# Optimization experiments

Hardware: AMD Instinct MI355X
Metric: run time of the kernel (lower is better)

## Reference

```python
import jax, jax.numpy as jnp
import numpy as np

MIN_PS = 4
MAX_PS = 16


def _enforce(mb):
    # mb: (L,) bool candidate boundaries (merge_signal < 0.7-quantile)
    # Faithful re-implementation of _enforce_patch_size_constraints:
    # walk boundaries left->right, skip segments < MIN_PS (start not advanced),
    # accept otherwise, and insert ceil(ps/MAX_PS)-1 evenly spaced splits for
    # oversized segments. seq_len-1 is always appended as a candidate.
    L = mb.shape[0]
    pos = jnp.arange(L, dtype=jnp.int32)
    cand = mb | (pos == L - 1)

    def fwd_step(start, inp):
        p, is_c = inp
        ps = p - start
        acc = is_c & (ps >= MIN_PS)
        k = jnp.where(acc, (ps + MAX_PS - 1) // MAX_PS, jnp.int32(1))
        sz = jnp.maximum(jnp.where(acc, ps // k, jnp.int32(1)), 1)
        new_start = jnp.where(acc, p, start)
        return new_start, (acc, start, sz, k)

    _, (acc, seg_start, sz, k) = jax.lax.scan(fwd_step, jnp.int32(0), (pos, cand))

    # Reverse scan: propagate each accepted boundary's (start, split_size, num_splits)
    # back to the interior positions of its segment so splits can be placed in parallel.
    def rev_step(carry, inp):
        a, s, z, kk = inp
        cs, cz, ck, cv = carry
        out = (cs, cz, ck, cv)
        ncarry = (jnp.where(a, s, cs), jnp.where(a, z, cz), jnp.where(a, kk, ck), cv | a)
        return ncarry, out

    init = (jnp.int32(0), jnp.int32(1), jnp.int32(1), jnp.bool_(False))
    _, (fs, fz, fk, fv) = jax.lax.scan(rev_step, init, (acc, seg_start, sz, k), reverse=True)
    r = pos - fs
    j = r // fz
    split = fv & (r > 0) & (r % fz == 0) & (j >= 1) & (j <= fk - 1)
    return acc | split


def reference(x, attention_mask, W1, b1, W2, b2, Wc, bc, Wb1, bb1, Wb2, bb2):
    B, L, D = x.shape
    # content scorer: Linear -> ReLU -> Linear -> Sigmoid
    content = jax.nn.sigmoid(jax.nn.relu(x @ W1 + b1) @ W2 + b2)[..., 0]  # (B, L)
    # grouped Conv1d(d, d//2, k=3, pad=1, groups=d//4)
    xc = jnp.transpose(x, (0, 2, 1))  # (B, D, L)
    pf = jax.lax.conv_general_dilated(xc, Wc, (1,), ((1, 1),),
                                      feature_group_count=D // 4,
                                      dimension_numbers=('NCH', 'OIH', 'NCH'))
    pf = jnp.transpose(pf + bc[None, :, None], (0, 2, 1))  # (B, L, D//2)
    comb = jnp.concatenate([x, pf], axis=-1)
    bscore = jax.nn.sigmoid(jax.nn.relu(comb @ Wb1 + bb1) @ Wb2 + bb2)[..., 0]  # (B, L)
    signal = content * (1.0 - bscore) * attention_mask
    thr = jnp.quantile(signal, 0.7, axis=1, keepdims=True)
    mb = signal < thr
    new_b = jax.vmap(_enforce)(mb)  # (B, L) bool, new_b[:,0] is always False

    # segment id per token = inclusive cumsum of boundaries
    seg = jnp.cumsum(new_b.astype(jnp.int32), axis=1)
    seg_flat = (seg + jnp.arange(B, dtype=jnp.int32)[:, None] * L).reshape(-1)
    NS = B * L
    xm = x * attention_mask[..., None]
    e = jnp.sum(xm * xm, axis=-1).reshape(-1)  # softmax logits = ||token||^2
    m = jax.ops.segment_max(e, seg_flat, num_segments=NS)
    w = jnp.exp(e - m[seg_flat])
    denom = jax.ops.segment_sum(w, seg_flat, num_segments=NS)
    wn = w / denom[seg_flat]
    merged = jax.ops.segment_sum(xm.reshape(-1, D) * wn[:, None], seg_flat,
                                 num_segments=NS).reshape(B, L, D)
    # segment_boundaries: 1 for every segment except the first, zero padding
    n_last = seg[:, -1]
    p = jnp.arange(L)
    seg_bounds = ((p[None, :] >= 1) & (p[None, :] <= n_last[:, None])).astype(jnp.float32)
    return merged, seg_bounds


def setup_inputs() -> dict:
    key = jax.random.key(0)
    B, L, D = 4, 8192, 512
    ks = jax.random.split(key, 8)
    s = 0.02
    return {
        'x': jax.random.normal(ks[0], (B, L, D), jnp.float32),
        'attention_mask': jnp.ones((B, L), jnp.float32),
        'W1': jax.random.normal(ks[1], (D, D // 4), jnp.float32) * s,
        'b1': jnp.zeros((D // 4,), jnp.float32),
        'W2': jax.random.normal(ks[2], (D // 4, 1), jnp.float32) * s,
        'b2': jnp.zeros((1,), jnp.float32),
        'Wc': jax.random.normal(ks[3], (D // 2, 4, 3), jnp.float32) * s,
        'bc': jnp.zeros((D // 2,), jnp.float32),
        'Wb1': jax.random.normal(ks[4], (D + D // 2, D // 4), jnp.float32) * s,
        'bb1': jnp.zeros((D // 4,), jnp.float32),
        'Wb2': jax.random.normal(ks[5], (D // 4, 1), jnp.float32) * s,
        'bb2': jnp.zeros((1,), jnp.float32),
    }
```

## Files before the change

### kernel.cpp

```cpp
#include <hip/hip_runtime.h>
#include <math.h>

#define B_  4
#define L_  8192
#define D_  512
#define BL_ (B_*L_)
#define TOK 64
#define XS  68
#define KC  16
#define NCH (D_/KC)

__global__ __launch_bounds__(256, 2) void k_signal(
    const float* __restrict__ x, const float* __restrict__ mask,
    const float* __restrict__ W1, const float* __restrict__ b1,
    const float* __restrict__ W2, const float* __restrict__ b2,
    const float* __restrict__ Wc, const float* __restrict__ bc,
    const float* __restrict__ Wb1, const float* __restrict__ bb1,
    const float* __restrict__ Wb2, const float* __restrict__ bb2,
    float* __restrict__ signal, float* __restrict__ e,
    unsigned int* __restrict__ hist16,
    float* __restrict__ merged, float* __restrict__ bounds)
{
  __shared__ float ws1[KC][128];
  __shared__ float wsb[KC][128];
  __shared__ float wsp[8][128];
  __shared__ float xt[KC][XS];
  __shared__ float pf[8][XS];

  const int t   = threadIdx.x;
  const int blk = blockIdx.x;
  const int b   = blk >> 7;
  const int l0  = (blk & 127) << 6;
  const float* xb = x + (size_t)b * L_ * D_;

  const int jq = t & 31, tw = t >> 5;
  const int j0 = jq << 2, tok0 = tw << 3;

  const int stok = t >> 2, skk = t & 3;
  const int oo_c = t >> 5;
  const int m2   = (t & 31) << 1;
  const int cb_c = (oo_c >> 1) << 2;

  const int srow = t >> 5, sc4 = (t & 31) << 2;

  if (t < 16) {
    float4* bz = reinterpret_cast<float4*>(bounds + (size_t)b * L_ + l0);
    bz[t] = make_float4(0.f, 0.f, 0.f, 0.f);
  }
  float4* mz = reinterpret_cast<float4*>(merged + (size_t)(b * L_ + l0) * D_);

  float a1[8][4], a2[8][4];
#pragma unroll
  for (int i = 0; i < 8; ++i)
#pragma unroll
    for (int j = 0; j < 4; ++j) { a1[i][j] = 0.f; a2[i][j] = 0.f; }
  float esacc = 0.f;

  float4 r_w1a, r_w1b, r_wba, r_wbb, r_wp, r_xv, r_hv;
  float4 r_wc0, r_wc1, r_wc2;
  float  r_bc;

  auto LOAD = [&](int c) {
    const int kc = c << 4;
    r_w1a = *reinterpret_cast<const float4*>(W1  + (size_t)(kc + srow) * 128 + sc4);
    r_w1b = *reinterpret_cast<const float4*>(W1  + (size_t)(kc + 8 + srow) * 128 + sc4);
    r_wba = *reinterpret_cast<const float4*>(Wb1 + (size_t)(kc + srow) * 128 + sc4);
    r_wbb = *reinterpret_cast<const float4*>(Wb1 + (size_t)(kc + 8 + srow) * 128 + sc4);
    r_wp  = *reinterpret_cast<const float4*>(Wb1 + (size_t)(512 + (c << 3) + srow) * 128 + sc4);
    r_xv  = *reinterpret_cast<const float4*>(xb + (size_t)(l0 + stok) * D_ + kc + (skk << 2));
    if (t < 8) {
      const int hh = t >> 2, kk = t & 3;
      const int l = hh ? (l0 + TOK) : (l0 - 1);
      r_hv = make_float4(0.f, 0.f, 0.f, 0.f);
      if (l >= 0 && l < L_)
        r_hv = *reinterpret_cast<const float4*>(xb + (size_t)l * D_ + kc + (kk << 2));
    }
    const int o = (c << 3) + oo_c;
    const float* wcp = Wc + o * 12;
    r_wc0 = *reinterpret_cast<const float4*>(wcp);
    r_wc1 = *reinterpret_cast<const float4*>(wcp + 4);
    r_wc2 = *reinterpret_cast<const float4*>(wcp + 8);
    r_bc  = bc[o];
  };

  LOAD(0);

  for (int c = 0; c < NCH; ++c) {
    __syncthreads();

    *reinterpret_cast<float4*>(&ws1[srow][sc4])     = r_w1a;
    *reinterpret_cast<float4*>(&ws1[8 + srow][sc4]) = r_w1b;
    *reinterpret_cast<float4*>(&wsb[srow][sc4])     = r_wba;
    *reinterpret_cast<float4*>(&wsb[8 + srow][sc4]) = r_wbb;
    *reinterpret_cast<float4*>(&wsp[srow][sc4])     = r_wp;
    {
      const float4 v = r_xv;
      esacc = fmaf(v.x, v.x, esacc); esacc = fmaf(v.y, v.y, esacc);
      esacc = fmaf(v.z, v.z, esacc); esacc = fmaf(v.w, v.w, esacc);
      const int r = skk << 2;
      xt[r + 0][stok] = v.x; xt[r + 1][stok] = v.y;
      xt[r + 2][stok] = v.z; xt[r + 3][stok] = v.w;
    }
    if (t < 8) {
      const int hh = t >> 2, kk = t & 3;
      const int col = TOK + hh, r = kk << 2;
      xt[r + 0][col] = r_hv.x; xt[r + 1][col] = r_hv.y;
      xt[r + 2][col] = r_hv.z; xt[r + 3][col] = r_hv.w;
    }
    __syncthreads();

    float wcl[12];
    wcl[0] = r_wc0.x; wcl[1]  = r_wc0.y; wcl[2]  = r_wc0.z; wcl[3]  = r_wc0.w;
    wcl[4] = r_wc1.x; wcl[5]  = r_wc1.y; wcl[6]  = r_wc1.z; wcl[7]  = r_wc1.w;
    wcl[8] = r_wc2.x; wcl[9]  = r_wc2.y; wcl[10] = r_wc2.z; wcl[11] = r_wc2.w;
    const float bcv = r_bc;

    if (c + 1 < NCH) LOAD(c + 1);

    mz[(c << 8) + t] = make_float4(0.f, 0.f, 0.f, 0.f);

    {
      float pa = bcv, pb = bcv;
      const int tm1 = (m2 == 0) ? TOK : m2 - 1;
      const int tp2 = (m2 + 2 == TOK) ? TOK + 1 : m2 + 2;
#pragma unroll
      for (int i = 0; i < 4; ++i) {
        const float* row = &xt[cb_c + i][0];
        const float  xm1 = row[tm1];
        const float2 x01 = *reinterpret_cast<const float2*>(&row[m2]);
        const float  xp2 = row[tp2];
        pa = fmaf(xm1,   wcl[i * 3 + 0], pa);
        pa = fmaf(x01.x, wcl[i * 3 + 1], pa);
        pa = fmaf(x01.y, wcl[i * 3 + 2], pa);
        pb = fmaf(x01.x, wcl[i * 3 + 0], pb);
        pb = fmaf(x01.y, wcl[i * 3 + 1], pb);
        pb = fmaf(xp2,   wcl[i * 3 + 2], pb);
      }
      *reinterpret_cast<float2*>(&pf[oo_c][m2]) = make_float2(pa, pb);
    }

#pragma unroll 4
    for (int k = 0; k < KC; ++k) {
      const float4 w1 = *reinterpret_cast<const float4*>(&ws1[k][j0]);
      const float4 wb = *reinterpret_cast<const float4*>(&wsb[k][j0]);
      const float4 xa = *reinterpret_cast<const float4*>(&xt[k][tok0]);
      const float4 xc = *reinterpret_cast<const float4*>(&xt[k][tok0 + 4]);
      const float xs8[8] = {xa.x, xa.y, xa.z, xa.w, xc.x, xc.y, xc.z, xc.w};
#pragma unroll
      for (int i = 0; i < 8; ++i) {
        a1[i][0] = fmaf(xs8[i], w1.x, a1[i][0]);
        a1[i][1] = fmaf(xs8[i], w1.y, a1[i][1]);
        a1[i][2] = fmaf(xs8[i], w1.z, a1[i][2]);
        a1[i][3] = fmaf(xs8[i], w1.w, a1[i][3]);
        a2[i][0] = fmaf(xs8[i], wb.x, a2[i][0]);
        a2[i][1] = fmaf(xs8[i], wb.y, a2[i][1]);
        a2[i][2] = fmaf(xs8[i], wb.z, a2[i][2]);
        a2[i][3] = fmaf(xs8[i], wb.w, a2[i][3]);
      }
    }
    __syncthreads();

#pragma unroll 2
    for (int oo = 0; oo < 8; ++oo) {
      const float4 wp = *reinterpret_cast<const float4*>(&wsp[oo][j0]);
      const float4 pa4 = *reinterpret_cast<const float4*>(&pf[oo][tok0]);
      const float4 pb4 = *reinterpret_cast<const float4*>(&pf[oo][tok0 + 4]);
      const float ps8[8] = {pa4.x, pa4.y, pa4.z, pa4.w, pb4.x, pb4.y, pb4.z, pb4.w};
#pragma unroll
      for (int i = 0; i < 8; ++i) {
        a2[i][0] = fmaf(ps8[i], wp.x, a2[i][0]);
        a2[i][1] = fmaf(ps8[i], wp.y, a2[i][1]);
        a2[i][2] = fmaf(ps8[i], wp.z, a2[i][2]);
        a2[i][3] = fmaf(ps8[i], wp.w, a2[i][3]);
      }
    }
  }

  {
    float b1v[4], w2v[4], bbv[4], wv2[4];
#pragma unroll
    for (int jj = 0; jj < 4; ++jj) {
      b1v[jj] = b1[j0 + jj];  w2v[jj] = W2[j0 + jj];
      bbv[jj] = bb1[j0 + jj]; wv2[jj] = Wb2[j0 + jj];
    }
    const float bias2 = b2[0], biasb2 = bb2[0];
#pragma unroll
    for (int i = 0; i < 8; ++i) {
      float p1 = 0.f, p2 = 0.f;
#pragma unroll
      for (int jj = 0; jj < 4; ++jj) {
        const float h1 = a1[i][jj] + b1v[jj];
        if (h1 > 0.f) p1 = fmaf(h1, w2v[jj], p1);
        const float h2 = a2[i][jj] + bbv[jj];
        if (h2 > 0.f) p2 = fmaf(h2, wv2[jj], p2);
      }
#pragma unroll
      for (int off = 1; off < 32; off <<= 1) {
        p1 += __shfl_xor(p1, off, 64);
        p2 += __shfl_xor(p2, off, 64);
      }
      if (jq == 0) {
        const int gi = b * L_ + l0 + tok0 + i;
        const float content = 1.f / (1.f + expf(-(p1 + bias2)));
        const float bscore  = 1.f / (1.f + expf(-(p2 + biasb2)));
        const float s = content * (1.f - bscore) * mask[gi];
        signal[gi] = s;
        const unsigned int u = __float_as_uint(s);
        const unsigned int key = (u & 0x80000000u) ? ~u : (u | 0x80000000u);
        const unsigned int bb16 = key >> 16;
        atomicAdd(&hist16[((unsigned)b << 16) | ((bb16 & 63u) << 10) | (bb16 >> 6)], 1u);
      }
    }
  }

  {
    float es = esacc;
    es += __shfl_xor(es, 1, 64);
    es += __shfl_xor(es, 2, 64);
    if (skk == 0) {
      const int gi = b * L_ + l0 + stok;
      const float m = mask[gi];
      e[gi] = m * m * es;
    }
  }
}

__device__ __forceinline__ int chain_sim(unsigned long long w, int from) {
  int last = -1;
  while (from < 64) {
    const unsigned long long m = w & (~0ull << from);
    if (m == 0ull) break;
    const int p = __ffsll(m) - 1;
    last = p;
    from = p + 4;
  }
  return last;
}

__global__ __launch_bounds__(1024) void k_select(
    const float* __restrict__ signal, const unsigned int* __restrict__ hist16,
    int* __restrict__ starts, int* __restrict__ nlast)
{
  __shared__ unsigned int bins[4][256];
  __shared__ unsigned int sel_prefix;
  __shared__ int sel_rank;
  __shared__ int sel_tt, sel_rr;
  __shared__ unsigned int wpart[16];
  __shared__ float sh_thr;
  __shared__ unsigned int wmin[16];
  __shared__ int wcnt[16];
  __shared__ unsigned long long cw[128];
  __shared__ unsigned char nb[L_];
  __shared__ signed char tbl[128][4];
  __shared__ int st_in[128];
  __shared__ int offs[257];

  const int b = blockIdx.x, t = threadIdx.x;
  const int wv = t >> 6, lane = t & 63;
  const float* s = signal + b * L_;
  const unsigned int* hb = hist16 + ((unsigned)b << 16);

  float val[8];
  unsigned int key[8];
#pragma unroll
  for (int i = 0; i < 8; ++i) {
    val[i] = s[(i << 10) + t];
    const unsigned int u = __float_as_uint(val[i]);
    key[i] = (u & 0x80000000u) ? ~u : (u | 0x80000000u);
  }

  unsigned int tsum = 0;
#pragma unroll 8
  for (int i = 0; i < 64; ++i) tsum += hb[(i << 10) | t];
  {
    unsigned int run = tsum;
#pragma unroll
    for (int off = 1; off < 64; off <<= 1) {
      const unsigned int v = __shfl_up(run, off, 64);
      if (lane >= off) run += v;
    }
    if (lane == 63) wpart[wv] = run;
    __syncthreads();
    unsigned int wadd = 0;
    for (int g = 0; g < wv; ++g) wadd += wpart[g];
    run += wadd;
    const unsigned int excl = run - tsum;
    const int r = 5733;
    if (r >= (int)excl && r < (int)run) { sel_tt = t; sel_rr = r - (int)excl; }
    __syncthreads();
    if (t < 64) {
      const int tt = sel_tt, rr = sel_rr;
      const unsigned int cnt = hb[(t << 10) | tt];
      unsigned int irun = cnt;
#pragma unroll
      for (int off = 1; off < 64; off <<= 1) {
        const unsigned int v = __shfl_up(irun, off, 64);
        if (t >= off) irun += v;
      }
      const unsigned int iexcl = irun - cnt;
      if (rr >= (int)iexcl && rr < (int)irun) {
        sel_prefix = ((unsigned int)tt << 6) | (unsigned int)t;
        sel_rank   = rr - (int)iexcl;
      }
    }
    __syncthreads();
  }

  for (int round = 2; round < 4; ++round) {
    reinterpret_cast<unsigned int*>(bins)[t] = 0u;
    __syncthreads();
    const unsigned int pre = sel_prefix;
    const int shift = 24 - 8 * round;
#pragma unroll
    for (int i = 0; i < 8; ++i) {
      if ((key[i] >> (shift + 8)) == pre)
        atomicAdd(&bins[t >> 8][(key[i] >> shift) & 255u], 1u);
    }
    __syncthreads();
    if (t < 256)
      bins[0][t] = bins[0][t] + bins[1][t] + bins[2][t] + bins[3][t];
    __syncthreads();
    if (t < 64) {
      const unsigned int c0 = bins[0][(t << 2) + 0], c1 = bins[0][(t << 2) + 1];
      const unsigned int c2 = bins[0][(t << 2) + 2], c3 = bins[0][(t << 2) + 3];
      const unsigned int lsum = c0 + c1 + c2 + c3;
      unsigned int run = lsum;
#pragma unroll
      for (int off = 1; off < 64; off <<= 1) {
        const unsigned int v = __shfl_up(run, off, 64);
        if (t >= off) run += v;
      }
      const int r = sel_rank;
      if (r >= (int)(run - lsum) && r < (int)run) {
        int rr = r - (int)(run - lsum);
        unsigned int cbin;
        if (rr < (int)c0) { cbin = 0; }
        else if (rr < (int)(c0 + c1)) { cbin = 1; rr -= (int)c0; }
        else if (rr < (int)(c0 + c1 + c2)) { cbin = 2; rr -= (int)(c0 + c1); }
        else { cbin = 3; rr -= (int)(c0 + c1 + c2); }
        sel_rank = rr;
        sel_prefix = (pre << 8) | ((unsigned int)(t << 2) | cbin);
      }
    }
    __syncthreads();
  }
  const unsigned int k0 = sel_prefix;

  {
    int cle = 0;
    unsigned int mgt = 0xFFFFFFFFu;
#pragma unroll
    for (int i = 0; i < 8; ++i) {
      if (key[i] <= k0) ++cle;
      else mgt = min(mgt, key[i]);
    }
#pragma unroll
    for (int off = 1; off < 64; off <<= 1) {
      cle += __shfl_xor(cle, off, 64);
      mgt = min(mgt, (unsigned int)__shfl_xor((int)mgt, off, 64));
    }
    if (lane == 0) { wcnt[wv] = cle; wmin[wv] = mgt; }
    __syncthreads();
    if (t == 0) {
      int C = 0; unsigned int M = 0xFFFFFFFFu;
      for (int g = 0; g < 16; ++g) { C += wcnt[g]; M = min(M, wmin[g]); }
      const unsigned int k1 = (C >= 5735) ? k0 : M;
      const unsigned int u0 = (k0 & 0x80000000u) ? (k0 & 0x7fffffffu) : ~k0;
      const unsigned int u1 = (k1 & 0x80000000u) ? (k1 & 0x7fffffffu) : ~k1;
      const float v0 = __uint_as_float(u0);
      const float v1 = __uint_as_float(u1);
      const float g = 0.7f * 8191.0f - 5733.0f;
      sh_thr = v0 + g * (v1 - v0);
    }
    __syncthreads();
  }
  const float thr = sh_thr;

#pragma unroll
  for (int i = 0; i < 8; ++i) {
    const unsigned long long m = __ballot(val[i] < thr);
    if (lane == 0) cw[(i << 4) + wv] = m;
  }
  {
    const int base = t << 3;
#pragma unroll
    for (int i = 0; i < 8; ++i) nb[base + i] = 0;
  }
  __syncthreads();
  if (t == 0) cw[127] |= (1ull << 63);
  __syncthreads();

  if (t < 512) {
    const int blk = t >> 2, cls = t & 3;
    tbl[blk][cls] = (signed char)chain_sim(cw[blk], cls);
  }
  __syncthreads();

  if (t == 0) {
    int st = 0;
    for (int blk = 0; blk < 128; ++blk) {
      const int bs = blk << 6;
      st_in[blk] = st;
      int pl;
      if (blk == 0) {
        pl = chain_sim(cw[0], 4);
      } else {
        int off = st + 4 - bs;
        if (off < 0) off = 0;
        pl = tbl[blk][off];
      }
      if (pl >= 0) st = bs + pl;
    }
  }
  __syncthreads();

  if (t < 128) {
    const int bs = t << 6;
    const unsigned long long w = cw[t];
    int st = st_in[t];
    int from = st + 4 - bs;
    if (from < 0) from = 0;
    while (from < 64) {
      const unsigned long long m = w & (~0ull << from);
      if (m == 0ull) break;
      const int p_rel = __ffsll(m) - 1;
      const int p = bs + p_rel;
      nb[p] = 1;
      const int ps = p - st;
      const int k = (ps + 15) >> 4;
      if (k > 1) {
        int sz = ps / k; if (sz < 1) sz = 1;
        for (int j = 1; j < k; ++j) nb[st + j * sz] = 1;
      }
      st = p;
      from = p_rel + 4;
    }
  }
  __syncthreads();

  int ls = 0, run2 = 0;
  if (t < 256) {
    const int base = t << 5;
    for (int i = 0; i < 32; ++i) ls += nb[base + i];
    run2 = ls;
#pragma unroll
    for (int off = 1; off < 64; off <<= 1) {
      const int v = __shfl_up(run2, off, 64);
      if ((t & 63) >= off) run2 += v;
    }
    if ((t & 63) == 63) wcnt[t >> 6] = run2;
  }
  __syncthreads();
  if (t < 256) {
    const int w = t >> 6;
    int addb = 0;
    if (w > 0) addb += wcnt[0];
    if (w > 1) addb += wcnt[1];
    if (w > 2) addb += wcnt[2];
    offs[t] = addb + run2 - ls;
    if (t == 255) offs[256] = addb + run2;
  }
  __syncthreads();
  if (t < 256) {
    const int base = t << 5;
    int rn = offs[t];
    for (int i = 0; i < 32; ++i) {
      rn += nb[base + i];
      if (nb[base + i]) starts[b * L_ + rn] = base + i;
    }
  }
  if (t == 0) { starts[b * L_ + 0] = 0; nlast[b] = offs[256]; }
}

__global__ __launch_bounds__(256) void k_merge(const float* __restrict__ x,
    const float* __restrict__ mask, const float* __restrict__ e,
    const int* __restrict__ starts, const int* __restrict__ nlast,
    float* __restrict__ merged, float* __restrict__ bounds)
{
  const int idx = (blockIdx.x << 2) + (threadIdx.x >> 6);
  const int b   = idx >> 13;
  const int sid = idx & (L_ - 1);
  const int n = nlast[b];
  if (sid > n) return;
  const int lane = threadIdx.x & 63;
  if (lane == 0 && sid >= 1)
    bounds[(size_t)b * L_ + sid] = 1.0f;
  const int c0 = lane << 3;
  float* o = merged + (size_t)(b * L_ + sid) * D_ + c0;
  const int t0 = starts[b * L_ + sid];
  const int t1 = (sid < n) ? starts[b * L_ + sid + 1] : L_;
  const int len = t1 - t0;
  const float* eb = e + b * L_;

  float acc[8] = {0,0,0,0,0,0,0,0};

  if (len <= 64) {
    const float ev = (lane < len) ? eb[t0 + lane] : -INFINITY;
    float mx = ev;
#pragma unroll
    for (int off = 1; off < 64; off <<= 1)
      mx = fmaxf(mx, __shfl_xor(mx, off, 64));
    const float ex = expf(ev - mx);
    float den = ex;
#pragma unroll
    for (int off = 1; off < 64; off <<= 1)
      den += __shfl_xor(den, off, 64);
    const float mk = (lane < len) ? mask[b * L_ + t0 + lane] : 0.f;
    const float scl = (ex / den) * mk;

    const float* xr = x + (size_t)(b * L_ + t0) * D_ + c0;
    float4 u0 = reinterpret_cast<const float4*>(xr)[0];
    float4 u1 = reinterpret_cast<const float4*>(xr)[1];
    for (int r = 0; r < len; ++r) {
      float4 n0, n1;
      if (r + 1 < len) {
        const float* xn = xr + (size_t)(r + 1) * D_;
        n0 = reinterpret_cast<const float4*>(xn)[0];
        n1 = reinterpret_cast<const float4*>(xn)[1];
      }
      const float sc = __shfl(scl, r, 64);
      acc[0] = fmaf(sc, u0.x, acc[0]); acc[1] = fmaf(sc, u0.y, acc[1]);
      acc[2] = fmaf(sc, u0.z, acc[2]); acc[3] = fmaf(sc, u0.w, acc[3]);
      acc[4] = fmaf(sc, u1.x, acc[4]); acc[5] = fmaf(sc, u1.y, acc[5]);
      acc[6] = fmaf(sc, u1.z, acc[6]); acc[7] = fmaf(sc, u1.w, acc[7]);
      u0 = n0; u1 = n1;
    }
  } else {
    float mx = -INFINITY;
    for (int p = t0; p < t1; ++p) mx = fmaxf(mx, eb[p]);
    float den = 0.f;
    for (int p = t0; p < t1; ++p) den += expf(eb[p] - mx);
    for (int p = t0; p < t1; ++p) {
      const float wn = expf(eb[p] - mx) / den;
      const float sc = wn * mask[b * L_ + p];
      const float* xr = x + ((size_t)(b * L_ + p)) * D_ + c0;
      const float4 u0 = reinterpret_cast<const float4*>(xr)[0];
      const float4 u1 = reinterpret_cast<const float4*>(xr)[1];
      acc[0] = fmaf(sc, u0.x, acc[0]); acc[1] = fmaf(sc, u0.y, acc[1]);
      acc[2] = fmaf(sc, u0.z, acc[2]); acc[3] = fmaf(sc, u0.w, acc[3]);
      acc[4] = fmaf(sc, u1.x, acc[4]); acc[5] = fmaf(sc, u1.y, acc[5]);
      acc[6] = fmaf(sc, u1.z, acc[6]); acc[7] = fmaf(sc, u1.w, acc[7]);
    }
  }
  reinterpret_cast<float4*>(o)[0] = make_float4(acc[0], acc[1], acc[2], acc[3]);
  reinterpret_cast<float4*>(o)[1] = make_float4(acc[4], acc[5], acc[6], acc[7]);
}

extern "C" void kernel_launch(void* const* d_in, const int* in_sizes, int n_in,
                              void* d_out, int out_size, void* d_ws, size_t ws_size,
                              hipStream_t stream) {
  (void)in_sizes; (void)n_in; (void)out_size; (void)ws_size;
  const float* x    = (const float*)d_in[0];
  const float* mask = (const float*)d_in[1];
  const float* W1   = (const float*)d_in[2];
  const float* b1   = (const float*)d_in[3];
  const float* W2   = (const float*)d_in[4];
  const float* b2   = (const float*)d_in[5];
  const float* Wc   = (const float*)d_in[6];
  const float* bc   = (const float*)d_in[7];
  const float* Wb1  = (const float*)d_in[8];
  const float* bb1  = (const float*)d_in[9];
  const float* Wb2  = (const float*)d_in[10];
  const float* bb2  = (const float*)d_in[11];

  float* merged = (float*)d_out;
  float* bounds = (float*)d_out + (size_t)BL_ * D_;

  char* ws = (char*)d_ws;
  float*        signal = (float*)(ws);
  float*        e      = (float*)(ws + (size_t)BL_ * 4);
  int*          starts = (int*)  (ws + (size_t)BL_ * 8);
  int*          nlast  = (int*)  (ws + (size_t)BL_ * 12);
  unsigned int* hist16 = (unsigned int*)(ws + (size_t)BL_ * 12 + 1024);

  hipMemsetAsync(hist16, 0, (size_t)B_ * 65536 * sizeof(unsigned int), stream);
  k_signal<<<BL_ / TOK, 256, 0, stream>>>(x, mask, W1, b1, W2, b2, Wc, bc,
                                          Wb1, bb1, Wb2, bb2, signal, e,
                                          hist16, merged, bounds);
  k_select<<<B_, 1024, 0, stream>>>(signal, hist16, starts, nlast);
  k_merge<<<BL_ / 4, 256, 0, stream>>>(x, mask, e, starts, nlast, merged, bounds);
}
```

Baseline: 292.1 us.

## Parallelize segment-start chaining with a wavefront prefix scan of transfer functions

Replaces the serial 128-block loop run by thread 0, which carried the segment start across 64-position blocks, with a parallel scan. Each block's behaviour is encoded as a 4-entry transfer function packed into 64 bits, and these are composed with shuffle-based prefix composition across two wavefronts. The aim is to remove a single-thread serial dependency chain from the selection kernel. In exchange it adds extra shuffles, a more intricate composition rule and an additional barrier.

Measured after the change: 291.8 us. No clear change (-0.1%).

```diff
diff --git a/kernel.cpp b/kernel.cpp
--- a/kernel.cpp
+++ b/kernel.cpp
@@ -237,6 +237,26 @@
   return last;
 }
 
+__device__ __forceinline__ unsigned long long compose_fn(
+    unsigned long long g, unsigned long long f, int lobase) {
+  unsigned long long h = 0ull;
+  const int bs = lobase << 6;
+#pragma unroll
+  for (int c = 0; c < 4; ++c) {
+    const unsigned int p = (unsigned int)((g >> (c * 16)) & 0xFFFFu);
+    unsigned int q;
+    if (p == 0xFFFFu) {
+      q = (unsigned int)(f & 0xFFFFu);
+    } else {
+      int cls2 = (int)p + 4 - bs; if (cls2 < 0) cls2 = 0;
+      const unsigned int r = (unsigned int)((f >> (cls2 * 16)) & 0xFFFFu);
+      q = (r == 0xFFFFu) ? p : r;
+    }
+    h |= (unsigned long long)q << (c * 16);
+  }
+  return h;
+}
+
 __global__ __launch_bounds__(1024) void k_select(
     const float* __restrict__ signal, const unsigned int* __restrict__ hist16,
     int* __restrict__ starts, int* __restrict__ nlast)
@@ -250,6 +270,7 @@
   __shared__ unsigned int wmin[16];
   __shared__ int wcnt[16];
   __shared__ unsigned long long cw[128];
+  __shared__ unsigned long long sh_w0;
   __shared__ unsigned char nb[L_];
   __shared__ signed char tbl[128][4];
   __shared__ int st_in[128];
@@ -396,20 +417,40 @@
   }
   __syncthreads();
 
-  if (t == 0) {
-    int st = 0;
-    for (int blk = 0; blk < 128; ++blk) {
-      const int bs = blk << 6;
-      st_in[blk] = st;
-      int pl;
-      if (blk == 0) {
-        pl = chain_sim(cw[0], 4);
+  {
+    unsigned long long ffn = 0ull;
+    int lo = t;
+    if (t < 128) {
+      if (t == 0) {
+        const int p = chain_sim(cw[0], 4);
+        const unsigned long long e = (p >= 0) ? (unsigned long long)(unsigned int)p
+                                              : 0xFFFFull;
+        ffn = e | (e << 16) | (e << 32) | (e << 48);
       } else {
-        int off = st + 4 - bs;
-        if (off < 0) off = 0;
-        pl = tbl[blk][off];
-      }
-      if (pl >= 0) st = bs + pl;
+#pragma unroll
+        for (int c = 0; c < 4; ++c) {
+          const int p = tbl[t][c];
+          const unsigned long long ent =
+              (p >= 0) ? (unsigned long long)(unsigned int)((t << 6) + p)
+                       : 0xFFFFull;
+          ffn |= ent << (c * 16);
+        }
+      }
+      const int l7 = t & 63;
+#pragma unroll
+      for (int off = 1; off < 64; off <<= 1) {
+        const unsigned long long g = __shfl_up(ffn, off, 64);
+        const int glo = __shfl_up(lo, off, 64);
+        if (l7 >= off) { ffn = compose_fn(g, ffn, lo); lo = glo; }
+      }
+      if (t == 63) sh_w0 = ffn;
+    }
+    __syncthreads();
+    if (t >= 64 && t < 128) ffn = compose_fn(sh_w0, ffn, lo);
+    if (t == 0) st_in[0] = 0;
+    if (t < 127) {
+      const unsigned int p = (unsigned int)(ffn & 0xFFFFu);
+      st_in[t + 1] = (p == 0xFFFFu) ? 0 : (int)p;
     }
   }
   __syncthreads();
```
